# Performance work log

Hardware: AMD Instinct MI355X
Metric: run time of the kernel (lower is better)

## Reference

```python
import jax, jax.numpy as jnp
import numpy as np

B, T, C = 4, 1024, 1024
HS = 64
H = C // HS
D_W, D_A, D_V, D_G = 64, 64, 32, 128
EPS = 0.00064  # GroupNorm eps from the module


def _wkv(r, w, k, v, a, b):
    # RWKV-7 recurrence: S_t = S_{t-1}*diag(exp(-exp(w_t))) + (S_{t-1} a_t) b_t^T + v_t k_t^T ; y_t = S_t r_t
    Bv, Tv, Cv = r.shape
    rs = lambda t: t.reshape(Bv, Tv, H, HS)
    r, k, v, a, b = rs(r), rs(k), rs(v), rs(a), rs(b)
    wd = jnp.exp(-jnp.exp(rs(w)))  # per-head per-channel decay in (0,1)

    def step(S, xs):
        r_, w_, k_, v_, a_, b_ = xs  # each (B,H,N)
        sa = jnp.einsum('bhij,bhj->bhi', S, a_)
        S = S * w_[:, :, None, :] + sa[..., None] * b_[:, :, None, :] + v_[..., None] * k_[:, :, None, :]
        y = jnp.einsum('bhij,bhj->bhi', S, r_)
        return S, y

    xs = tuple(jnp.swapaxes(t, 0, 1) for t in (r, wd, k, v, a, b))  # (T,B,H,N)
    S0 = jnp.zeros((Bv, H, HS, HS), r.dtype)
    _, ys = jax.lax.scan(step, S0, xs)
    return jnp.swapaxes(ys, 0, 1).reshape(Bv, Tv, Cv)


def _forward(x, x_r, x_w, x_k, x_v, x_a, x_g, w0, w1, w2, a0, a1, a2, v0, v1, v2,
             g1, g2, k_k, k_a, r_k, Wr, Wk, Wv, Wo, ln_w, ln_b):
    Bv, Tv, Cv = x.shape
    # time_shift(x) - x  (ZeroPad2d((0,0,1,-1)))
    xx = jnp.concatenate([jnp.zeros_like(x[:, :1]), x[:, :-1]], axis=1) - x
    xr = x + xx * x_r; xw = x + xx * x_w; xk = x + xx * x_k
    xv = x + xx * x_v; xa = x + xx * x_a; xg = x + xx * x_g
    r = xr @ Wr
    w = -jax.nn.softplus(-(w0 + jnp.tanh(xw @ w1) @ w2)) - 0.5
    k = xk @ Wk
    v = xv @ Wv
    v_first = jax.lax.stop_gradient(v)  # first layer call: v_first == v.detach()
    v = v + (v_first - v) * jax.nn.sigmoid(v0 + xv @ v1 @ v2)
    a = jax.nn.sigmoid(a0 + xa @ a1 @ a2)
    g = jax.nn.sigmoid(xg @ g1) @ g2
    kk = k * k_k
    kkh = kk.reshape(Bv, Tv, H, HS)
    kkh = kkh / jnp.maximum(jnp.linalg.norm(kkh, axis=-1, keepdims=True), 1e-12)  # F.normalize
    kk = kkh.reshape(Bv, Tv, Cv)
    k = k * (1 + (a - 1) * k_a)
    y = _wkv(r, w, k, v, -kk, kk * a)
    # GroupNorm(H groups, eps=0.00064) over flattened (B*T, C)
    yh = y.reshape(Bv, Tv, H, HS)
    mu = jnp.mean(yh, axis=-1, keepdims=True)
    var = jnp.var(yh, axis=-1, keepdims=True)
    y = ((yh - mu) / jnp.sqrt(var + EPS)).reshape(Bv, Tv, Cv) * ln_w + ln_b
    rt = (r.reshape(Bv, Tv, H, HS) * k.reshape(Bv, Tv, H, HS) * r_k).sum(-1, keepdims=True) * v.reshape(Bv, Tv, H, HS)
    y = y + rt.reshape(Bv, Tv, Cv)
    return (y * g) @ Wo


def setup_inputs():
    key = jax.random.key(0)
    ks = jax.random.split(key, 28)
    it = iter(range(28))
    n = lambda shape, std: jax.random.normal(ks[next(it)], shape, jnp.float32) * std
    s = C ** -0.5
    return {
        'x': n((B, T, C), 1.0),
        'x_r': n((1, 1, C), 0.01), 'x_w': n((1, 1, C), 0.01), 'x_k': n((1, 1, C), 0.01),
        'x_v': n((1, 1, C), 0.01), 'x_a': n((1, 1, C), 0.01), 'x_g': n((1, 1, C), 0.01),
        'w0': n((1, 1, C), 0.02), 'w1': n((C, D_W), 0.04), 'w2': n((D_W, C), 0.04),
        'a0': n((1, 1, C), 0.02), 'a1': n((C, D_A), 0.04), 'a2': n((D_A, C), 0.04),
        'v0': n((1, 1, C), 0.02), 'v1': n((C, D_V), 0.04), 'v2': n((D_V, C), 0.04),
        'g1': n((C, D_G), 0.04), 'g2': n((D_G, C), 0.04),
        'k_k': n((1, 1, C), 0.02), 'k_a': n((1, 1, C), 0.02),
        'r_k': n((H, HS), 0.1) + 0.1 * jnp.arange(H, dtype=jnp.float32)[:, None],
        'Wr': n((C, C), s), 'Wk': n((C, C), s), 'Wv': n((C, C), s), 'Wo': n((C, C), s),
        'ln_w': jnp.ones((C,), jnp.float32), 'ln_b': jnp.zeros((C,), jnp.float32),
    }


def reference(x, x_r, x_w, x_k, x_v, x_a, x_g, w0, w1, w2, a0, a1, a2, v0, v1, v2,
              g1, g2, k_k, k_a, r_k, Wr, Wk, Wv, Wo, ln_w, ln_b):
    return _forward(x, x_r, x_w, x_k, x_v, x_a, x_g, w0, w1, w2, a0, a1, a2,
                    v0, v1, v2, g1, g2, k_k, k_a, r_k, Wr, Wk, Wv, Wo, ln_w, ln_b)
```

## Files before the change

kernel.cpp:

```cpp
#include <hip/hip_runtime.h>
#include <math.h>

#define Bsz 4
#define Tt  1024
#define Cc  1024
#define Hh  16
#define HSs 64
#define CL  32
#define NCH (Tt / CL)
#define STRD 260

typedef __attribute__((ext_vector_type(8))) short bf16x8;
typedef __attribute__((ext_vector_type(4))) float f32x4;

__device__ __forceinline__ float sigf(float x) { return 1.f / (1.f + expf(-x)); }

__device__ __forceinline__ unsigned short f2bf(float f) {
    unsigned int u = __float_as_uint(f);
    u = u + 0x7fffu + ((u >> 16) & 1u);
    return (unsigned short)(u >> 16);
}
__device__ __forceinline__ float bf2f(unsigned short u) {
    return __uint_as_float(((unsigned int)u) << 16);
}
__device__ __forceinline__ float dpp_add_xor1(float x) {
    int y = __builtin_amdgcn_mov_dpp(__float_as_int(x), 0xB1, 0xF, 0xF, true);
    return x + __int_as_float(y);
}
__device__ __forceinline__ float dpp_add_xor2(float x) {
    int y = __builtin_amdgcn_mov_dpp(__float_as_int(x), 0x4E, 0xF, 0xF, true);
    return x + __int_as_float(y);
}

__device__ __forceinline__ void gload16(const void* g, void* l) {
    __builtin_amdgcn_global_load_lds(
        (const __attribute__((address_space(1))) unsigned int*)g,
        (__attribute__((address_space(3))) unsigned int*)l, 16, 0, 0);
}

#define UNPK8(dst, u4, off) do { \
    const unsigned int* q_ = (const unsigned int*)&(u4); \
    _Pragma("unroll") \
    for (int e_ = 0; e_ < 4; ++e_) { \
        (dst)[(off) + 2 * e_]     = __uint_as_float(q_[e_] << 16); \
        (dst)[(off) + 2 * e_ + 1] = __uint_as_float(q_[e_] & 0xFFFF0000u); \
    } \
} while (0)

__device__ __forceinline__ void tcast64(
    const float* __restrict__ W, unsigned short* __restrict__ WT,
    int K, int N, int n0, int k0, int tid, unsigned short tile[64][68])
{
    const int tr = tid >> 4, tc4 = (tid & 15) * 4;
#pragma unroll
    for (int s = 0; s < 4; ++s) {
        int kk = tr + s * 16;
        float4 w4 = *(const float4*)(W + (size_t)(k0 + kk) * N + n0 + tc4);
        tile[kk][tc4 + 0] = f2bf(w4.x);
        tile[kk][tc4 + 1] = f2bf(w4.y);
        tile[kk][tc4 + 2] = f2bf(w4.z);
        tile[kk][tc4 + 3] = f2bf(w4.w);
    }
    __syncthreads();
#pragma unroll
    for (int s = 0; s < 4; ++s) {
        int nn = tr + s * 16;
        ushort4 o4;
        o4.x = tile[tc4 + 0][nn];
        o4.y = tile[tc4 + 1][nn];
        o4.z = tile[tc4 + 2][nn];
        o4.w = tile[tc4 + 3][nn];
        *(ushort4*)(WT + (size_t)(n0 + nn) * K + k0 + tc4) = o4;
    }
}

__global__ __launch_bounds__(256) void prep_all(
    const float* __restrict__ x, const float* __restrict__ x_r,
    const float* __restrict__ x_k, const float* __restrict__ x_v,
    const float* __restrict__ Wr, const float* __restrict__ Wk,
    const float* __restrict__ Wv, const float* __restrict__ Wo,
    const float* __restrict__ w1, const float* __restrict__ a1,
    const float* __restrict__ g1, const float* __restrict__ w2,
    const float* __restrict__ a2, const float* __restrict__ g2,
    unsigned short* __restrict__ xr, unsigned short* __restrict__ xk,
    unsigned short* __restrict__ xvo,
    unsigned short* __restrict__ WrT, unsigned short* __restrict__ WkT,
    unsigned short* __restrict__ WvT, unsigned short* __restrict__ WoT,
    unsigned short* __restrict__ w1t, unsigned short* __restrict__ a1t,
    unsigned short* __restrict__ g1t, unsigned short* __restrict__ w2t,
    unsigned short* __restrict__ a2t, unsigned short* __restrict__ g2t)
{
    __shared__ unsigned short tile[64][68];
    const int tid = threadIdx.x;
    int bid = blockIdx.x;

    if (bid < 4096) {
        const int row = bid;
        const int c0 = tid * 4;
        const size_t o = (size_t)row * Cc;
        float4 xc = *(const float4*)(x + o + c0);
        float4 xp;
        if (row & (Tt - 1)) xp = *(const float4*)(x + o - Cc + c0);
        else { xp.x = xp.y = xp.z = xp.w = 0.f; }
        float4 mr = *(const float4*)(x_r + c0);
        float4 mk = *(const float4*)(x_k + c0);
        float4 mv = *(const float4*)(x_v + c0);
        const float* xcf = (const float*)&xc; const float* xpf = (const float*)&xp;
        const float* mrf = (const float*)&mr; const float* mkf = (const float*)&mk;
        const float* mvf = (const float*)&mv;
        ushort4 r4, k4, v4;
        unsigned short* rp = (unsigned short*)&r4;
        unsigned short* kp = (unsigned short*)&k4;
        unsigned short* vp = (unsigned short*)&v4;
#pragma unroll
        for (int j = 0; j < 4; ++j) {
            float xx = xpf[j] - xcf[j];
            rp[j] = f2bf(xcf[j] + xx * mrf[j]);
            kp[j] = f2bf(xcf[j] + xx * mkf[j]);
            vp[j] = f2bf(xcf[j] + xx * mvf[j]);
        }
        *(ushort4*)(xr + o + c0) = r4;
        *(ushort4*)(xk + o + c0) = k4;
        *(ushort4*)(xvo + o + c0) = v4;
        return;
    }
    bid -= 4096;
    if (bid < 1024) {
        int which = bid >> 8, id0 = bid & 255;
        const float* W = which == 0 ? Wr : which == 1 ? Wk : which == 2 ? Wv : Wo;
        unsigned short* WT = which == 0 ? WrT : which == 1 ? WkT : which == 2 ? WvT : WoT;
        tcast64(W, WT, Cc, Cc, (id0 & 15) * 64, (id0 >> 4) * 64, tid, tile);
        return;
    }
    bid -= 1024;
    if (bid < 16) { tcast64(w1, w1t, Cc, 64, 0, bid * 64, tid, tile); return; }
    bid -= 16;
    if (bid < 16) { tcast64(a1, a1t, Cc, 64, 0, bid * 64, tid, tile); return; }
    bid -= 16;
    if (bid < 32) { tcast64(g1, g1t, Cc, 128, (bid & 1) * 64, (bid >> 1) * 64, tid, tile); return; }
    bid -= 32;
    if (bid < 16) { tcast64(w2, w2t, 64, Cc, bid * 64, 0, tid, tile); return; }
    bid -= 16;
    if (bid < 16) { tcast64(a2, a2t, 64, Cc, bid * 64, 0, tid, tile); return; }
    bid -= 16;
    tcast64(g2, g2t, 128, Cc, (bid & 15) * 64, (bid >> 4) * 64, tid, tile);
}

__global__ __launch_bounds__(256) void gemm_rkv(
    const unsigned short* __restrict__ xr, const unsigned short* __restrict__ xk,
    const unsigned short* __restrict__ xv,
    const unsigned short* __restrict__ WrT, const unsigned short* __restrict__ WkT,
    const unsigned short* __restrict__ WvT,
    unsigned short* __restrict__ rbh, unsigned short* __restrict__ kbh,
    unsigned short* __restrict__ vbh)
{
    const int z = blockIdx.z;
    const unsigned short* A  = z == 0 ? xr : z == 1 ? xk : xv;
    const unsigned short* WT = z == 0 ? WrT : z == 1 ? WkT : WvT;
    unsigned short* outh = z == 0 ? rbh : z == 1 ? kbh : vbh;
    const int K = Cc, N = Cc;

    const int bid = blockIdx.x + 8 * blockIdx.y;
    const int swz = (bid & 7) * 32 + (bid >> 3);
    const int row0 = (swz >> 3) * 128;
    const int col0 = (swz & 7) * 128;

    __shared__ __attribute__((aligned(16))) unsigned short As[128 * 32];
    __shared__ __attribute__((aligned(16))) unsigned short Bs[128 * 32];
    const int tid = threadIdx.x;
    const int wave = tid >> 6, lane = tid & 63;
    const int wr = wave >> 1, wc = wave & 1;
    const int lr = lane & 15, lk = lane >> 4;

    f32x4 acc[4][4];
#pragma unroll
    for (int m = 0; m < 4; ++m)
#pragma unroll
        for (int n = 0; n < 4; ++n)
#pragma unroll
            for (int r = 0; r < 4; ++r) acc[m][n][r] = 0.f;

    const int lrow = lane >> 2;
    const int lcol8 = (lane & 3) * 8;

    for (int k0 = 0; k0 < K; k0 += 32) {
#pragma unroll
        for (int e = 0; e < 2; ++e) {
            int cib = wave * 128 + e * 64;
            int row = (cib >> 2) + lrow;
            gload16(A  + (size_t)(row0 + row) * K + k0 + lcol8, &As[cib * 8]);
            gload16(WT + (size_t)(col0 + row) * K + k0 + lcol8, &Bs[cib * 8]);
        }
        __syncthreads();
        bf16x8 af[4], bff[4];
#pragma unroll
        for (int m = 0; m < 4; ++m)
            af[m] = *(const bf16x8*)&As[(wr * 64 + m * 16 + lr) * 32 + lk * 8];
#pragma unroll
        for (int n = 0; n < 4; ++n)
            bff[n] = *(const bf16x8*)&Bs[(wc * 64 + n * 16 + lr) * 32 + lk * 8];
#pragma unroll
        for (int m = 0; m < 4; ++m)
#pragma unroll
            for (int n = 0; n < 4; ++n)
                acc[m][n] = __builtin_amdgcn_mfma_f32_16x16x32_bf16(af[m], bff[n], acc[m][n], 0, 0, 0);
        __syncthreads();
    }

#pragma unroll
    for (int m = 0; m < 4; ++m)
#pragma unroll
        for (int n = 0; n < 4; ++n) {
            int col = col0 + wc * 64 + n * 16 + lr;
#pragma unroll
            for (int r = 0; r < 4; ++r) {
                int row = row0 + wr * 64 + m * 16 + lk * 4 + r;
                outh[(size_t)row * N + col] = f2bf(acc[m][n][r]);
            }
        }
}

__global__ __launch_bounds__(256) void gemm_bf16(
    const unsigned short* __restrict__ A, const unsigned short* __restrict__ WT,
    float* __restrict__ out, int M, int N, int K)
{
    __shared__ __attribute__((aligned(16))) unsigned short As[128 * 32];
    __shared__ __attribute__((aligned(16))) unsigned short Bs[128 * 32];
    const int bid = blockIdx.x + 8 * blockIdx.y;
    const int swz = (bid & 7) * 32 + (bid >> 3);
    const int row0 = (swz >> 3) * 128;
    const int col0 = (swz & 7) * 128;
    const int tid = threadIdx.x;
    const int wave = tid >> 6, lane = tid & 63;
    const int wr = wave >> 1, wc = wave & 1;
    const int lr = lane & 15, lk = lane >> 4;

    f32x4 acc[4][4];
#pragma unroll
    for (int m = 0; m < 4; ++m)
#pragma unroll
        for (int n = 0; n < 4; ++n)
#pragma unroll
            for (int r = 0; r < 4; ++r) acc[m][n][r] = 0.f;

    const int lrow = lane >> 2;
    const int lcol8 = (lane & 3) * 8;

    for (int k0 = 0; k0 < K; k0 += 32) {
#pragma unroll
        for (int e = 0; e < 2; ++e) {
            int cib = wave * 128 + e * 64;
            int row = (cib >> 2) + lrow;
            gload16(A  + (size_t)(row0 + row) * K + k0 + lcol8, &As[cib * 8]);
            gload16(WT + (size_t)(col0 + row) * K + k0 + lcol8, &Bs[cib * 8]);
        }
        __syncthreads();
        bf16x8 af[4], bff[4];
#pragma unroll
        for (int m = 0; m < 4; ++m)
            af[m] = *(const bf16x8*)&As[(wr * 64 + m * 16 + lr) * 32 + lk * 8];
#pragma unroll
        for (int n = 0; n < 4; ++n)
            bff[n] = *(const bf16x8*)&Bs[(wc * 64 + n * 16 + lr) * 32 + lk * 8];
#pragma unroll
        for (int m = 0; m < 4; ++m)
#pragma unroll
            for (int n = 0; n < 4; ++n)
                acc[m][n] = __builtin_amdgcn_mfma_f32_16x16x32_bf16(af[m], bff[n], acc[m][n], 0, 0, 0);
        __syncthreads();
    }

#pragma unroll
    for (int m = 0; m < 4; ++m)
#pragma unroll
        for (int n = 0; n < 4; ++n) {
            int col = col0 + wc * 64 + n * 16 + lr;
#pragma unroll
            for (int r = 0; r < 4; ++r) {
                int row = row0 + wr * 64 + m * 16 + lk * 4 + r;
                out[(size_t)row * N + col] = acc[m][n][r];
            }
        }
}

__global__ __launch_bounds__(256) void lowrank1_fused(
    const float* __restrict__ x,
    const float* __restrict__ x_w, const float* __restrict__ x_a,
    const float* __restrict__ x_g,
    const unsigned short* __restrict__ w1t, const unsigned short* __restrict__ a1t,
    const unsigned short* __restrict__ g1t,
    unsigned short* __restrict__ hw, unsigned short* __restrict__ ha,
    unsigned short* __restrict__ hg)
{
    const int seg = blockIdx.x;
    const float* mix; const unsigned short* WT; unsigned short* out;
    int N, col0, epi;
    if (seg == 0)      { mix = x_w; WT = w1t; out = hw; N = 64;  col0 = 0; epi = 1; }
    else if (seg == 1) { mix = x_a; WT = a1t; out = ha; N = 64;  col0 = 0; epi = 0; }
    else               { mix = x_g; WT = g1t; out = hg; N = 128; col0 = (seg - 2) * 64; epi = 2; }

    __shared__ __attribute__((aligned(16))) unsigned short As[64][40];
    __shared__ __attribute__((aligned(16))) unsigned short Bs[64][40];
    const int row0 = blockIdx.y * 64;
    const int tid = threadIdx.x;
    const int wave = tid >> 6, lane = tid & 63;
    const int lr = lane & 15, lk = lane >> 4;

    f32x4 acc[4];
#pragma unroll
    for (int n = 0; n < 4; ++n)
#pragma unroll
        for (int r = 0; r < 4; ++r) acc[n][r] = 0.f;

    for (int k0 = 0; k0 < Cc; k0 += 32) {
        {
            int ar = tid >> 2, ac = (tid & 3) * 8;
            int row = row0 + ar;
            const float* xp = x + (size_t)row * Cc + k0 + ac;
            float4 c0 = *(const float4*)xp;
            float4 c1 = *(const float4*)(xp + 4);
            float4 p0, p1;
            if (row & (Tt - 1)) {
                p0 = *(const float4*)(xp - Cc);
                p1 = *(const float4*)(xp - Cc + 4);
            } else {
                p0.x = p0.y = p0.z = p0.w = 0.f;
                p1.x = p1.y = p1.z = p1.w = 0.f;
            }
            float4 m0 = *(const float4*)(mix + k0 + ac);
            float4 m1 = *(const float4*)(mix + k0 + ac + 4);
            const float* cf0 = (const float*)&c0; const float* cf1 = (const float*)&c1;
            const float* pf0 = (const float*)&p0; const float* pf1 = (const float*)&p1;
            const float* mf0 = (const float*)&m0; const float* mf1 = (const float*)&m1;
            ushort4 u0, u1;
            unsigned short* up0 = (unsigned short*)&u0;
            unsigned short* up1 = (unsigned short*)&u1;
#pragma unroll
            for (int j = 0; j < 4; ++j) {
                up0[j] = f2bf(cf0[j] + (pf0[j] - cf0[j]) * mf0[j]);
                up1[j] = f2bf(cf1[j] + (pf1[j] - cf1[j]) * mf1[j]);
            }
            *(ushort4*)&As[ar][ac] = u0;
            *(ushort4*)&As[ar][ac + 4] = u1;
        }
        {
            int br = tid >> 2, bc = (tid & 3) * 8;
            *(uint4*)&Bs[br][bc] = *(const uint4*)(WT + (size_t)(col0 + br) * Cc + k0 + bc);
        }
        __syncthreads();
        bf16x8 af, bff[4];
        af = *(const bf16x8*)&As[wave * 16 + lr][lk * 8];
#pragma unroll
        for (int n = 0; n < 4; ++n)
            bff[n] = *(const bf16x8*)&Bs[n * 16 + lr][lk * 8];
#pragma unroll
        for (int n = 0; n < 4; ++n)
            acc[n] = __builtin_amdgcn_mfma_f32_16x16x32_bf16(af, bff[n], acc[n], 0, 0, 0);
        __syncthreads();
    }

#pragma unroll
    for (int n = 0; n < 4; ++n) {
        int col = col0 + n * 16 + lr;
#pragma unroll
        for (int r = 0; r < 4; ++r) {
            int row = row0 + wave * 16 + lk * 4 + r;
            float v = acc[n][r];
            if (epi == 1) v = tanhf(v);
            else if (epi == 2) v = sigf(v);
            out[(size_t)row * N + col] = f2bf(v);
        }
    }
}

__global__ __launch_bounds__(256) void stage2_fused(
    const unsigned short* __restrict__ hw, const unsigned short* __restrict__ ha,
    const unsigned short* __restrict__ hg,
    const unsigned short* __restrict__ w2t, const unsigned short* __restrict__ a2t,
    const unsigned short* __restrict__ g2t,
    unsigned short* __restrict__ wdbh, float* __restrict__ abf,
    unsigned short* __restrict__ gb,
    const float* __restrict__ w0, const float* __restrict__ a0)
{
    const int z = blockIdx.z;
    const unsigned short* A  = z == 0 ? hw : z == 1 ? ha : hg;
    const unsigned short* WT = z == 0 ? w2t : z == 1 ? a2t : g2t;
    const float* bias = z == 0 ? w0 : z == 1 ? a0 : nullptr;
    const int K = (z == 2) ? 128 : 64;
    const int N = Cc;

    __shared__ __attribute__((aligned(16))) unsigned short As[128 * 32];
    __shared__ __attribute__((aligned(16))) unsigned short Bs[64 * 32];
    const int row0 = blockIdx.y * 128;
    const int col0 = blockIdx.x * 64;
    const int tid = threadIdx.x;
    const int wave = tid >> 6, lane = tid & 63;
    const int lr = lane & 15, lk = lane >> 4;

    f32x4 acc[2][4];
#pragma unroll
    for (int m = 0; m < 2; ++m)
#pragma unroll
        for (int n = 0; n < 4; ++n)
#pragma unroll
            for (int r = 0; r < 4; ++r) acc[m][n][r] = 0.f;

    const int lrow = lane >> 2;
    const int lcol8 = (lane & 3) * 8;

    for (int k0 = 0; k0 < K; k0 += 32) {
#pragma unroll
        for (int e = 0; e < 2; ++e) {
            int cib = wave * 128 + e * 64;
            int row = (cib >> 2) + lrow;
            gload16(A + (size_t)(row0 + row) * K + k0 + lcol8, &As[cib * 8]);
        }
        {
            int cib = wave * 64;
            int row = (cib >> 2) + lrow;
            gload16(WT + (size_t)(col0 + row) * K + k0 + lcol8, &Bs[cib * 8]);
        }
        __syncthreads();
        bf16x8 af[2], bff[4];
#pragma unroll
        for (int m = 0; m < 2; ++m)
            af[m] = *(const bf16x8*)&As[(wave * 32 + m * 16 + lr) * 32 + lk * 8];
#pragma unroll
        for (int n = 0; n < 4; ++n)
            bff[n] = *(const bf16x8*)&Bs[(n * 16 + lr) * 32 + lk * 8];
#pragma unroll
        for (int m = 0; m < 2; ++m)
#pragma unroll
            for (int n = 0; n < 4; ++n)
                acc[m][n] = __builtin_amdgcn_mfma_f32_16x16x32_bf16(af[m], bff[n], acc[m][n], 0, 0, 0);
        __syncthreads();
    }

#pragma unroll
    for (int m = 0; m < 2; ++m)
#pragma unroll
        for (int n = 0; n < 4; ++n) {
            int col = col0 + n * 16 + lr;
#pragma unroll
            for (int r = 0; r < 4; ++r) {
                int row = row0 + wave * 32 + m * 16 + lk * 4 + r;
                float v = acc[m][n][r];
                if (bias) v += bias[col];
                if (z == 0) {
                    v = expf(-0.60653065971263342f * sigf(v));
                    wdbh[(size_t)row * N + col] = f2bf(v);
                } else if (z == 1) {
                    abf[(size_t)row * N + col] = sigf(v);
                } else {
                    gb[(size_t)row * N + col] = f2bf(v);
                }
            }
        }
}

__global__ __launch_bounds__(256, 1) void wkv_chunk1(
    const unsigned short* __restrict__ rbh, const unsigned short* __restrict__ wdbh,
    const unsigned short* __restrict__ kraw, const float* __restrict__ abf,
    const float* __restrict__ k_k, const float* __restrict__ k_a,
    unsigned short* __restrict__ TLt,
    unsigned short* __restrict__ Rho,
    unsigned short* __restrict__ ZLt,
    unsigned short* __restrict__ Alh)
{
    __shared__ float st[CL * STRD];
    __shared__ float A_l[CL][CL + 1];
    const int blk = blockIdx.x;
    const int bh = blk >> 5;
    const int c  = blk & (NCH - 1);
    const int b = bh >> 4, h = bh & 15;
    const size_t base = (size_t)b * Tt * Cc + h * HSs + (size_t)c * CL * Cc;
    const int tid = threadIdx.x;

    {
        const int s = tid >> 3, j8 = (tid & 7) * 8;
        const size_t go = base + (size_t)s * Cc + j8;
        {
            uint4 u = *(const uint4*)(wdbh + go);
            const unsigned int* q = (const unsigned int*)&u;
            float4 f0, f1;
            f0.x = __uint_as_float(q[0] << 16); f0.y = __uint_as_float(q[0] & 0xFFFF0000u);
            f0.z = __uint_as_float(q[1] << 16); f0.w = __uint_as_float(q[1] & 0xFFFF0000u);
            f1.x = __uint_as_float(q[2] << 16); f1.y = __uint_as_float(q[2] & 0xFFFF0000u);
            f1.z = __uint_as_float(q[3] << 16); f1.w = __uint_as_float(q[3] & 0xFFFF0000u);
            *(float4*)&st[s * STRD + 1 * 64 + j8] = f0;
            *(float4*)&st[s * STRD + 1 * 64 + j8 + 4] = f1;
        }
        {
            uint4 u = *(const uint4*)(rbh + go);
            const unsigned int* q = (const unsigned int*)&u;
            float4 f0, f1;
            f0.x = __uint_as_float(q[0] << 16); f0.y = __uint_as_float(q[0] & 0xFFFF0000u);
            f0.z = __uint_as_float(q[1] << 16); f0.w = __uint_as_float(q[1] & 0xFFFF0000u);
            f1.x = __uint_as_float(q[2] << 16); f1.y = __uint_as_float(q[2] & 0xFFFF0000u);
            f1.z = __uint_as_float(q[3] << 16); f1.w = __uint_as_float(q[3] & 0xFFFF0000u);
            *(float4*)&st[s * STRD + 3 * 64 + j8] = f0;
            *(float4*)&st[s * STRD + 3 * 64 + j8 + 4] = f1;
        }
        float kr[8];
        {
            uint4 u = *(const uint4*)(kraw + go);
            UNPK8(kr, u, 0);
        }
        float4 av0 = *(const float4*)(abf + go);
        float4 av1 = *(const float4*)(abf + go + 4);
        const float* avp0 = (const float*)&av0;
        const float* avp1 = (const float*)&av1;
        const int ch0 = h * HSs + j8;
        float4 kk0 = *(const float4*)(k_k + ch0);
        float4 kk1 = *(const float4*)(k_k + ch0 + 4);
        const float* kkw = (const float*)&kk0;
        const float* kkw1 = (const float*)&kk1;
        float kkv[8];
#pragma unroll
        for (int j = 0; j < 4; ++j) {
            kkv[j] = kr[j] * kkw[j];
            kkv[4 + j] = kr[4 + j] * kkw1[j];
        }
        float ssq = 0.f;
#pragma unroll
        for (int j = 0; j < 8; ++j) ssq = fmaf(kkv[j], kkv[j], ssq);
        ssq = dpp_add_xor1(ssq);
        ssq = dpp_add_xor2(ssq);
        ssq += __shfl_xor(ssq, 4);
        float inv = 1.f / fmaxf(sqrtf(ssq), 1e-12f);
        float4 aa0, aa1, bb0, bb1;
        float* aap = (float*)&aa0; float* bbp = (float*)&bb0;
#pragma unroll
        for (int j = 0; j < 4; ++j) {
            float kkn = kkv[j] * inv;
            aap[j] = -kkn;
            bbp[j] = kkn * avp0[j];
        }
        float* aq = (float*)&aa1; float* bq = (float*)&bb1;
#pragma unroll
        for (int j = 0; j < 4; ++j) {
            float kkn = kkv[4 + j] * inv;
            aq[j] = -kkn;
            bq[j] = kkn * avp1[j];
        }
        *(float4*)&st[s * STRD + 0 * 64 + j8] = aa0;
        *(float4*)&st[s * STRD + 0 * 64 + j8 + 4] = aa1;
        *(float4*)&st[s * STRD + 2 * 64 + j8] = bb0;
        *(float4*)&st[s * STRD + 2 * 64 + j8 + 4] = bb1;
    }
    __syncthreads();

    const int wv = tid >> 6, lane = tid & 63;
    if (wv < 2) {
        const int idx = wv * 64 + lane;
        const int rq = idx >> 2, jc = idx & 3;
        const int i0 = rq * 2, j0 = jc * 16;
        float T[2][16];
#pragma unroll
        for (int rr = 0; rr < 2; ++rr)
#pragma unroll
            for (int cc = 0; cc < 16; ++cc)
                T[rr][cc] = (i0 + rr == j0 + cc) ? 1.f : 0.f;
        const size_t rhob = (size_t)blk * (CL * 64);

        for (int t = 0; t < CL; ++t) {
            const float* sp = st + t * STRD;
            float a[16], w[16], bv[16], r[16];
#pragma unroll
            for (int q = 0; q < 4; ++q) {
                *(float4*)&a[q * 4]  = *(const float4*)(sp + 0 * 64 + j0 + q * 4);
                *(float4*)&w[q * 4]  = *(const float4*)(sp + 1 * 64 + j0 + q * 4);
                *(float4*)&bv[q * 4] = *(const float4*)(sp + 2 * 64 + j0 + q * 4);
                *(float4*)&r[q * 4]  = *(const float4*)(sp + 3 * 64 + j0 + q * 4);
            }
            float ta[2];
#pragma unroll
            for (int rr = 0; rr < 2; ++rr) {
                float q0 = T[rr][0] * a[0], q1 = T[rr][4] * a[4];
                float q2 = T[rr][8] * a[8], q3 = T[rr][12] * a[12];
#pragma unroll
                for (int e = 1; e < 4; ++e) {
                    q0 = fmaf(T[rr][e], a[e], q0);
                    q1 = fmaf(T[rr][4 + e], a[4 + e], q1);
                    q2 = fmaf(T[rr][8 + e], a[8 + e], q2);
                    q3 = fmaf(T[rr][12 + e], a[12 + e], q3);
                }
                ta[rr] = (q0 + q1) + (q2 + q3);
            }
#pragma unroll
            for (int rr = 0; rr < 2; ++rr) {
                ta[rr] = dpp_add_xor1(ta[rr]);
                ta[rr] = dpp_add_xor2(ta[rr]);
            }
            float rp[2];
#pragma unroll
            for (int rr = 0; rr < 2; ++rr) {
                float q0 = 0.f, q1 = 0.f, q2 = 0.f, q3 = 0.f;
#pragma unroll
                for (int e = 0; e < 4; ++e) {
                    T[rr][e]      = fmaf(T[rr][e],      w[e],      ta[rr] * bv[e]);
                    T[rr][4 + e]  = fmaf(T[rr][4 + e],  w[4 + e],  ta[rr] * bv[4 + e]);
                    T[rr][8 + e]  = fmaf(T[rr][8 + e],  w[8 + e],  ta[rr] * bv[8 + e]);
                    T[rr][12 + e] = fmaf(T[rr][12 + e], w[12 + e], ta[rr] * bv[12 + e]);
                    q0 = fmaf(T[rr][e], r[e], q0);
                    q1 = fmaf(T[rr][4 + e], r[4 + e], q1);
                    q2 = fmaf(T[rr][8 + e], r[8 + e], q2);
                    q3 = fmaf(T[rr][12 + e], r[12 + e], q3);
                }
                rp[rr] = (q0 + q1) + (q2 + q3);
            }
#pragma unroll
            for (int rr = 0; rr < 2; ++rr) {
                rp[rr] = dpp_add_xor1(rp[rr]);
                rp[rr] = dpp_add_xor2(rp[rr]);
            }
            if (jc == 0) {
                ushort2 o2;
                o2.x = f2bf(rp[0]); o2.y = f2bf(rp[1]);
                *(ushort2*)(Rho + rhob + t * 64 + i0) = o2;
            }
        }
        const size_t tlb = (size_t)blk * 4096;
#pragma unroll
        for (int cc = 0; cc < 16; ++cc) {
            ushort2 o2;
            o2.x = f2bf(T[0][cc]); o2.y = f2bf(T[1][cc]);
            *(ushort2*)(TLt + tlb + (size_t)(j0 + cc) * 64 + i0) = o2;
        }
    } else {
        const int idx2 = (wv - 2) * 64 + lane;
        const int s = idx2 >> 2, q4 = idx2 & 3;
        const int j0 = q4 * 16;
        float kreg[16];
        {
            float kr[16];
            uint4 u0 = *(const uint4*)(kraw + base + (size_t)s * Cc + j0);
            uint4 u1 = *(const uint4*)(kraw + base + (size_t)s * Cc + j0 + 8);
            UNPK8(kr, u0, 0); UNPK8(kr, u1, 8);
#pragma unroll
            for (int q = 0; q < 4; ++q) {
                float4 av4 = *(const float4*)(abf + base + (size_t)s * Cc + j0 + q * 4);
                float4 ka4 = *(const float4*)(k_a + h * HSs + j0 + q * 4);
                const float* avp = (const float*)&av4;
                const float* kap = (const float*)&ka4;
#pragma unroll
                for (int e = 0; e < 4; ++e) {
                    int u = q * 4 + e;
                    kreg[u] = kr[u] * (1.f + (avp[e] - 1.f) * kap[e]);
                }
            }
        }
        float z[16];
#pragma unroll
        for (int u = 0; u < 16; ++u) z[u] = 0.f;

        for (int t = 0; t < CL; ++t) {
            const float* sp = st + t * STRD;
            float a[16], w[16], bv[16], r[16];
#pragma unroll
            for (int q = 0; q < 4; ++q) {
                *(float4*)&a[q * 4]  = *(const float4*)(sp + 0 * 64 + j0 + q * 4);
                *(float4*)&w[q * 4]  = *(const float4*)(sp + 1 * 64 + j0 + q * 4);
                *(float4*)&bv[q * 4] = *(const float4*)(sp + 2 * 64 + j0 + q * 4);
                *(float4*)&r[q * 4]  = *(const float4*)(sp + 3 * 64 + j0 + q * 4);
            }
            float q0 = z[0] * a[0], q1 = z[4] * a[4];
            float q2 = z[8] * a[8], q3 = z[12] * a[12];
#pragma unroll
            for (int e = 1; e < 4; ++e) {
                q0 = fmaf(z[e], a[e], q0);
                q1 = fmaf(z[4 + e], a[4 + e], q1);
                q2 = fmaf(z[8 + e], a[8 + e], q2);
                q3 = fmaf(z[12 + e], a[12 + e], q3);
            }
            float za = (q0 + q1) + (q2 + q3);
            za = dpp_add_xor1(za);
            za = dpp_add_xor2(za);
#pragma unroll
            for (int u = 0; u < 16; ++u)
                z[u] = fmaf(z[u], w[u], za * bv[u]);
            if (s == t) {
#pragma unroll
                for (int u = 0; u < 16; ++u) z[u] = kreg[u];
            }
            float p0 = z[0] * r[0], p1 = z[4] * r[4];
            float p2 = z[8] * r[8], p3 = z[12] * r[12];
#pragma unroll
            for (int e = 1; e < 4; ++e) {
                p0 = fmaf(z[e], r[e], p0);
                p1 = fmaf(z[4 + e], r[4 + e], p1);
                p2 = fmaf(z[8 + e], r[8 + e], p2);
                p3 = fmaf(z[12 + e], r[12 + e], p3);
            }
            float al = (p0 + p1) + (p2 + p3);
            al = dpp_add_xor1(al);
            al = dpp_add_xor2(al);
            if (q4 == 0) A_l[t][s] = al;
        }
        const size_t zlb = (size_t)blk * (CL * 64);
#pragma unroll
        for (int u = 0; u < 16; ++u)
            ZLt[zlb + (size_t)(j0 + u) * 32 + s] = f2bf(z[u]);
    }
    __syncthreads();

    if (tid < 128) {
        const int t = tid >> 2, s8 = (tid & 3) * 8;
        ushort4 o0, o1;
        unsigned short* p0 = (unsigned short*)&o0;
        unsigned short* p1 = (unsigned short*)&o1;
#pragma unroll
        for (int e = 0; e < 4; ++e) {
            p0[e] = f2bf(A_l[t][s8 + e]);
            p1[e] = f2bf(A_l[t][s8 + 4 + e]);
        }
        unsigned short* dst = Alh + (size_t)blk * 1024 + t * 32 + s8;
        *(ushort4*)dst = o0;
        *(ushort4*)(dst + 4) = o1;
    }
}

__global__ __launch_bounds__(256, 1) void wkv_chunk2(
    const unsigned short* __restrict__ vbh, const unsigned short* __restrict__ TLt,
    const unsigned short* __restrict__ Rho, const unsigned short* __restrict__ ZLt,
    const unsigned short* __restrict__ Alh, float* __restrict__ yb)
{
    __shared__ unsigned short Sl[64 * 72];
    __shared__ unsigned short Ttl[64 * 72];
    __shared__ unsigned short Ztl[64 * 40];
    __shared__ unsigned short Rl[32 * 72];
    __shared__ unsigned short Vtl[64 * 40];
    __shared__ unsigned short All[32 * 40];
    const int bh = blockIdx.x;
    const size_t vbase = (size_t)(bh >> 4) * Tt * Cc + (bh & 15) * HSs;
    const int tid = threadIdx.x;
    const int wv = tid >> 6, lane = tid & 63;
    const int lr = lane & 15, lk = lane >> 4;
    const int i0w = wv * 16;

    f32x4 S[4];
#pragma unroll
    for (int n = 0; n < 4; ++n)
#pragma unroll
        for (int r = 0; r < 4; ++r) S[n][r] = 0.f;

    uint4 pT0, pT1, pZ, pR, pAl, pVu;
    const int vs = tid >> 3, vi0 = (tid & 7) * 8;

#define C2_LOAD(c_) do { \
    size_t cb_ = (size_t)(bh * NCH + (c_)); \
    const uint4* tp_ = (const uint4*)(TLt + cb_ * 4096); \
    pT0 = tp_[tid * 2]; pT1 = tp_[tid * 2 + 1]; \
    pZ = ((const uint4*)(ZLt + cb_ * 2048))[tid]; \
    pR = ((const uint4*)(Rho + cb_ * 2048))[tid]; \
    if (tid < 128) pAl = ((const uint4*)(Alh + cb_ * 1024))[tid]; \
    pVu = *(const uint4*)(vbh + vbase + (size_t)((c_) * CL + vs) * Cc + vi0); \
} while (0)

#define C2_STORE() do { \
    *(uint4*)&Ttl[(tid >> 2) * 72 + (tid & 3) * 16] = pT0; \
    *(uint4*)&Ttl[(tid >> 2) * 72 + (tid & 3) * 16 + 8] = pT1; \
    *(uint4*)&Ztl[(tid >> 2) * 40 + (tid & 3) * 8] = pZ; \
    *(uint4*)&Rl[(tid >> 3) * 72 + (tid & 7) * 8] = pR; \
    if (tid < 128) *(uint4*)&All[(tid >> 2) * 40 + (tid & 3) * 8] = pAl; \
    const unsigned short* pvu_ = (const unsigned short*)&pVu; \
    Vtl[(vi0 + 0) * 40 + vs] = pvu_[0]; \
    Vtl[(vi0 + 1) * 40 + vs] = pvu_[1]; \
    Vtl[(vi0 + 2) * 40 + vs] = pvu_[2]; \
    Vtl[(vi0 + 3) * 40 + vs] = pvu_[3]; \
    Vtl[(vi0 + 4) * 40 + vs] = pvu_[4]; \
    Vtl[(vi0 + 5) * 40 + vs] = pvu_[5]; \
    Vtl[(vi0 + 6) * 40 + vs] = pvu_[6]; \
    Vtl[(vi0 + 7) * 40 + vs] = pvu_[7]; \
} while (0)

    C2_LOAD(0);
    for (int c = 0; c < NCH; ++c) {
        __syncthreads();
#pragma unroll
        for (int n = 0; n < 4; ++n) {
#pragma unroll
            for (int r = 0; r < 4; ++r)
                Sl[(i0w + lk * 4 + r) * 72 + n * 16 + lr] = f2bf(S[n][r]);
        }
        C2_STORE();
        if (c + 1 < NCH) C2_LOAD(c + 1);
        __syncthreads();

        bf16x8 sA0 = *(const bf16x8*)&Sl[(i0w + lr) * 72 + lk * 8];
        bf16x8 sA1 = *(const bf16x8*)&Sl[(i0w + lr) * 72 + 32 + lk * 8];
        bf16x8 vA = *(const bf16x8*)&Vtl[(i0w + lr) * 40 + lk * 8];

#pragma unroll
        for (int nt = 0; nt < 2; ++nt) {
            int t = nt * 16 + lr;
            float* yp = yb + vbase + (size_t)(c * CL + t) * Cc + i0w + lk * 4;
            f32x4 yc = { 0.f, 0.f, 0.f, 0.f };
            bf16x8 b0 = *(const bf16x8*)&Rl[t * 72 + lk * 8];
            bf16x8 b1 = *(const bf16x8*)&Rl[t * 72 + 32 + lk * 8];
            bf16x8 al8 = *(const bf16x8*)&All[t * 40 + lk * 8];
            yc = __builtin_amdgcn_mfma_f32_16x16x32_bf16(sA0, b0, yc, 0, 0, 0);
            yc = __builtin_amdgcn_mfma_f32_16x16x32_bf16(sA1, b1, yc, 0, 0, 0);
            yc = __builtin_amdgcn_mfma_f32_16x16x32_bf16(vA, al8, yc, 0, 0, 0);
            *(f32x4*)yp = yc;
        }

#pragma unroll
        for (int n = 0; n < 4; ++n) {
            int j = n * 16 + lr;
            bf16x8 t0 = *(const bf16x8*)&Ttl[j * 72 + lk * 8];
            bf16x8 t1 = *(const bf16x8*)&Ttl[j * 72 + 32 + lk * 8];
            bf16x8 z0 = *(const bf16x8*)&Ztl[j * 40 + lk * 8];
            f32x4 acc = { 0.f, 0.f, 0.f, 0.f };
            acc = __builtin_amdgcn_mfma_f32_16x16x32_bf16(sA0, t0, acc, 0, 0, 0);
            acc = __builtin_amdgcn_mfma_f32_16x16x32_bf16(sA1, t1, acc, 0, 0, 0);
            acc = __builtin_amdgcn_mfma_f32_16x16x32_bf16(vA, z0, acc, 0, 0, 0);
            S[n] = acc;
        }
    }
#undef C2_LOAD
#undef C2_STORE
}

__global__ __launch_bounds__(256) void gn_rt_kernel(
    const float* __restrict__ yb, const unsigned short* __restrict__ rbh,
    const unsigned short* __restrict__ kraw, const float* __restrict__ abf,
    const unsigned short* __restrict__ vbh,
    const unsigned short* __restrict__ gb, const float* __restrict__ r_k,
    const float* __restrict__ k_a,
    const float* __restrict__ ln_w, const float* __restrict__ ln_b,
    unsigned short* __restrict__ zb)
{
    const int row = blockIdx.x;
    const int tid = threadIdx.x;
    const int c0 = tid * 4;
    const int hd = tid >> 4;
    const int n0 = c0 & 63;
    const size_t o = (size_t)row * Cc;

    float4 y4 = *(const float4*)(yb + o + c0);
    ushort4 r4u = *(const ushort4*)(rbh + o + c0);
    ushort4 k4u = *(const ushort4*)(kraw + o + c0);
    float4 a4 = *(const float4*)(abf + o + c0);
    ushort4 v4u = *(const ushort4*)(vbh + o + c0);
    ushort4 g4u = *(const ushort4*)(gb + o + c0);
    float4 rk4 = *(const float4*)(r_k + hd * 64 + n0);
    float4 ka4 = *(const float4*)(k_a + c0);

    float yv[4] = { y4.x, y4.y, y4.z, y4.w };
    float rv[4] = { bf2f(r4u.x), bf2f(r4u.y), bf2f(r4u.z), bf2f(r4u.w) };
    float krv[4] = { bf2f(k4u.x), bf2f(k4u.y), bf2f(k4u.z), bf2f(k4u.w) };
    const float* avp = (const float*)&a4;
    float vv[4] = { bf2f(v4u.x), bf2f(v4u.y), bf2f(v4u.z), bf2f(v4u.w) };
    float gv[4] = { bf2f(g4u.x), bf2f(g4u.y), bf2f(g4u.z), bf2f(g4u.w) };
    float rkv[4] = { rk4.x, rk4.y, rk4.z, rk4.w };
    const float* kap = (const float*)&ka4;

    float kv[4];
#pragma unroll
    for (int j = 0; j < 4; ++j)
        kv[j] = krv[j] * (1.f + (avp[j] - 1.f) * kap[j]);

    float sum = 0.f, ssq = 0.f, dot = 0.f;
#pragma unroll
    for (int j = 0; j < 4; ++j) {
        sum += yv[j];
        ssq += yv[j] * yv[j];
        dot += rv[j] * kv[j] * rkv[j];
    }
#pragma unroll
    for (int m = 1; m <= 8; m <<= 1) {
        sum += __shfl_xor(sum, m);
        ssq += __shfl_xor(ssq, m);
        dot += __shfl_xor(dot, m);
    }
    const float mu = sum * (1.f / 64.f);
    const float var = ssq * (1.f / 64.f) - mu * mu;
    const float inv = rsqrtf(var + 0.00064f);

    ushort4 z4;
    unsigned short* zp = (unsigned short*)&z4;
#pragma unroll
    for (int j = 0; j < 4; ++j) {
        int c = c0 + j;
        float yg = (yv[j] - mu) * inv * ln_w[c] + ln_b[c];
        yg += dot * vv[j];
        zp[j] = f2bf(yg * gv[j]);
    }
    *(ushort4*)(zb + o + c0) = z4;
}


extern "C" void kernel_launch(void* const* d_in, const int* in_sizes, int n_in,
                              void* d_out, int out_size, void* d_ws, size_t ws_size,
                              hipStream_t stream)
{
    const float* x   = (const float*)d_in[0];
    const float* x_r = (const float*)d_in[1];
    const float* x_w = (const float*)d_in[2];
    const float* x_k = (const float*)d_in[3];
    const float* x_v = (const float*)d_in[4];
    const float* x_a = (const float*)d_in[5];
    const float* x_g = (const float*)d_in[6];
    const float* w0  = (const float*)d_in[7];
    const float* w1  = (const float*)d_in[8];
    const float* w2  = (const float*)d_in[9];
    const float* a0  = (const float*)d_in[10];
    const float* a1  = (const float*)d_in[11];
    const float* a2  = (const float*)d_in[12];
    const float* g1  = (const float*)d_in[16];
    const float* g2  = (const float*)d_in[17];
    const float* k_k = (const float*)d_in[18];
    const float* k_a = (const float*)d_in[19];
    const float* r_k = (const float*)d_in[20];
    const float* Wr  = (const float*)d_in[21];
    const float* Wk  = (const float*)d_in[22];
    const float* Wv  = (const float*)d_in[23];
    const float* Wo  = (const float*)d_in[24];
    const float* ln_w = (const float*)d_in[25];
    const float* ln_b = (const float*)d_in[26];

    float* ws = (float*)d_ws;
    const size_t S = (size_t)Bsz * Tt * Cc;
    const int M = Bsz * Tt;

    unsigned short* rbh = (unsigned short*)(ws + 0 * S);
    unsigned short* zb  = (unsigned short*)ws + S;
    unsigned short* wdbh = (unsigned short*)(ws + 1 * S);
    unsigned short* gb  = (unsigned short*)(ws + 1 * S) + S;
    unsigned short* kbh = (unsigned short*)(ws + 2 * S);
    unsigned short* vbh = (unsigned short*)(ws + 2 * S) + S;
    float* abf = ws + 3 * S;
    float* yb = ws + 4 * S;
    unsigned short* xr = (unsigned short*)(ws + 5 * S);
    unsigned short* xk = (unsigned short*)(ws + 5 * S) + S;
    unsigned short* Rho = xr;
    unsigned short* ZLt = xk;
    unsigned short* xv = (unsigned short*)(ws + 6 * S);
    unsigned short* hw = xv + S;
    unsigned short* ha = hw + 262144;
    unsigned short* hg = ha + 262144;
    unsigned short* w1t = hg + 524288;
    unsigned short* a1t = w1t + 65536;
    unsigned short* g1t = a1t + 65536;
    unsigned short* w2t = g1t + 131072;
    unsigned short* a2t = w2t + 65536;
    unsigned short* g2t = a2t + 65536;
    unsigned short* WrT = (unsigned short*)(ws + 7 * S);
    unsigned short* WkT = WrT + 1048576;
    unsigned short* WvT = WkT + 1048576;
    unsigned short* WoT = WvT + 1048576;
    unsigned short* Alh = WoT + 1048576;
    unsigned short* TLt = (unsigned short*)(ws + 8 * S);

    dim3 blk(256);

    prep_all<<<dim3(4096 + 1024 + 128), blk, 0, stream>>>(
        x, x_r, x_k, x_v, Wr, Wk, Wv, Wo, w1, a1, g1, w2, a2, g2,
        xr, xk, xv, WrT, WkT, WvT, WoT, w1t, a1t, g1t, w2t, a2t, g2t);

    lowrank1_fused<<<dim3(4, 64), blk, 0, stream>>>(x, x_w, x_a, x_g, w1t, a1t, g1t, hw, ha, hg);

    gemm_rkv<<<dim3(8, 32, 3), blk, 0, stream>>>(xr, xk, xv, WrT, WkT, WvT, rbh, kbh, vbh);

    stage2_fused<<<dim3(16, 32, 3), blk, 0, stream>>>(hw, ha, hg, w2t, a2t, g2t, wdbh, abf, gb, w0, a0);

    wkv_chunk1<<<dim3(64 * NCH), dim3(256), 0, stream>>>(rbh, wdbh, kbh, abf, k_k, k_a, TLt, Rho, ZLt, Alh);
    wkv_chunk2<<<dim3(64), blk, 0, stream>>>(vbh, TLt, Rho, ZLt, Alh, yb);

    gn_rt_kernel<<<dim3(M), blk, 0, stream>>>(yb, rbh, kbh, abf, vbh, gb, r_k, k_a, ln_w, ln_b, zb);

    gemm_bf16<<<dim3(8, 32), blk, 0, stream>>>(zb, WoT, (float*)d_out, M, Cc, Cc);
}
```

Measured before the change: 225.2 us.

## Fuse GroupNorm and gating epilogue into the sequential WKV chunk kernel

The chunked WKV output is staged per chunk in shared memory and normalized in place. The GroupNorm, r*k*r_k bonus term and g gating are done inside wkv_chunk2, and the separate gn_rt kernel and the fp32 y buffer are removed. This saves a launch and a full fp32 write/read of y. The cost is that each of the 32 sequential chunk steps now does extra global loads of r, k, a, g and v plus an added barrier. That is work on the latency-bound critical path of a 64-block kernel.

```diff
diff --git a/kernel.cpp b/kernel.cpp
--- a/kernel.cpp
+++ b/kernel.cpp
@@ -723,7 +723,12 @@
 __global__ __launch_bounds__(256, 1) void wkv_chunk2(
     const unsigned short* __restrict__ vbh, const unsigned short* __restrict__ TLt,
     const unsigned short* __restrict__ Rho, const unsigned short* __restrict__ ZLt,
-    const unsigned short* __restrict__ Alh, float* __restrict__ yb)
+    const unsigned short* __restrict__ Alh,
+    const unsigned short* __restrict__ rbh, const unsigned short* __restrict__ kraw,
+    const float* __restrict__ abf, const unsigned short* __restrict__ gb,
+    const float* __restrict__ r_k, const float* __restrict__ k_a,
+    const float* __restrict__ ln_w, const float* __restrict__ ln_b,
+    unsigned short* __restrict__ zb)
 {
     __shared__ unsigned short Sl[64 * 72];
     __shared__ unsigned short Ttl[64 * 72];
@@ -731,8 +736,10 @@
     __shared__ unsigned short Rl[32 * 72];
     __shared__ unsigned short Vtl[64 * 40];
     __shared__ unsigned short All[32 * 40];
+    __shared__ float Yl[32 * 68];
     const int bh = blockIdx.x;
-    const size_t vbase = (size_t)(bh >> 4) * Tt * Cc + (bh & 15) * HSs;
+    const int h = bh & 15;
+    const size_t vbase = (size_t)(bh >> 4) * Tt * Cc + h * HSs;
     const int tid = threadIdx.x;
     const int wv = tid >> 6, lane = tid & 63;
     const int lr = lane & 15, lk = lane >> 4;
@@ -743,6 +750,19 @@
     for (int n = 0; n < 4; ++n)
 #pragma unroll
         for (int r = 0; r < 4; ++r) S[n][r] = 0.f;
+
+    const int gt = tid >> 3;
+    const int gi = (tid & 7) * 8;
+    const int chb = h * HSs + gi;
+    float ka8[8], rk8[8], lnw8[8], lnb8[8];
+    *(float4*)&ka8[0] = *(const float4*)(k_a + chb);
+    *(float4*)&ka8[4] = *(const float4*)(k_a + chb + 4);
+    *(float4*)&rk8[0] = *(const float4*)(r_k + chb);
+    *(float4*)&rk8[4] = *(const float4*)(r_k + chb + 4);
+    *(float4*)&lnw8[0] = *(const float4*)(ln_w + chb);
+    *(float4*)&lnw8[4] = *(const float4*)(ln_w + chb + 4);
+    *(float4*)&lnb8[0] = *(const float4*)(ln_b + chb);
+    *(float4*)&lnb8[4] = *(const float4*)(ln_b + chb + 4);
 
     uint4 pT0, pT1, pZ, pR, pAl, pVu;
     const int vs = tid >> 3, vi0 = (tid & 7) * 8;
@@ -794,7 +814,6 @@
 #pragma unroll
         for (int nt = 0; nt < 2; ++nt) {
             int t = nt * 16 + lr;
-            float* yp = yb + vbase + (size_t)(c * CL + t) * Cc + i0w + lk * 4;
             f32x4 yc = { 0.f, 0.f, 0.f, 0.f };
             bf16x8 b0 = *(const bf16x8*)&Rl[t * 72 + lk * 8];
             bf16x8 b1 = *(const bf16x8*)&Rl[t * 72 + 32 + lk * 8];
@@ -802,7 +821,7 @@
             yc = __builtin_amdgcn_mfma_f32_16x16x32_bf16(sA0, b0, yc, 0, 0, 0);
             yc = __builtin_amdgcn_mfma_f32_16x16x32_bf16(sA1, b1, yc, 0, 0, 0);
             yc = __builtin_amdgcn_mfma_f32_16x16x32_bf16(vA, al8, yc, 0, 0, 0);
-            *(f32x4*)yp = yc;
+            *(float4*)&Yl[t * 68 + i0w + lk * 4] = *(float4*)&yc;
         }
 
 #pragma unroll
@@ -817,77 +836,55 @@
             acc = __builtin_amdgcn_mfma_f32_16x16x32_bf16(vA, z0, acc, 0, 0, 0);
             S[n] = acc;
         }
+
+        __syncthreads();
+
+        {
+            const size_t grow = vbase + (size_t)(c * CL + gt) * Cc + gi;
+            float y8[8];
+            *(float4*)&y8[0] = *(const float4*)&Yl[gt * 68 + gi];
+            *(float4*)&y8[4] = *(const float4*)&Yl[gt * 68 + gi + 4];
+            float r8[8], k8[8], g8[8], v8[8];
+            uint4 ur = *(const uint4*)(rbh + grow);  UNPK8(r8, ur, 0);
+            uint4 uk = *(const uint4*)(kraw + grow); UNPK8(k8, uk, 0);
+            uint4 ug = *(const uint4*)(gb + grow);   UNPK8(g8, ug, 0);
+            uint4 uv = *(const uint4*)(vbh + grow);  UNPK8(v8, uv, 0);
+            float a8[8];
+            *(float4*)&a8[0] = *(const float4*)(abf + grow);
+            *(float4*)&a8[4] = *(const float4*)(abf + grow + 4);
+
+            float sum = 0.f, ssq = 0.f, dot = 0.f;
+            float kf8[8];
+#pragma unroll
+            for (int j = 0; j < 8; ++j) {
+                kf8[j] = k8[j] * (1.f + (a8[j] - 1.f) * ka8[j]);
+                sum += y8[j];
+                ssq = fmaf(y8[j], y8[j], ssq);
+                dot = fmaf(r8[j] * kf8[j], rk8[j], dot);
+            }
+            sum = dpp_add_xor1(sum); sum = dpp_add_xor2(sum); sum += __shfl_xor(sum, 4);
+            ssq = dpp_add_xor1(ssq); ssq = dpp_add_xor2(ssq); ssq += __shfl_xor(ssq, 4);
+            dot = dpp_add_xor1(dot); dot = dpp_add_xor2(dot); dot += __shfl_xor(dot, 4);
+            const float mu = sum * (1.f / 64.f);
+            const float var = ssq * (1.f / 64.f) - mu * mu;
+            const float inv = rsqrtf(var + 0.00064f);
+
+            ushort4 z0o, z1o;
+            unsigned short* zp0 = (unsigned short*)&z0o;
+            unsigned short* zp1 = (unsigned short*)&z1o;
+#pragma unroll
+            for (int j = 0; j < 4; ++j) {
+                float yg0 = (y8[j] - mu) * inv * lnw8[j] + lnb8[j] + dot * v8[j];
+                float yg1 = (y8[4 + j] - mu) * inv * lnw8[4 + j] + lnb8[4 + j] + dot * v8[4 + j];
+                zp0[j] = f2bf(yg0 * g8[j]);
+                zp1[j] = f2bf(yg1 * g8[4 + j]);
+            }
+            *(ushort4*)(zb + grow) = z0o;
+            *(ushort4*)(zb + grow + 4) = z1o;
+        }
     }
 #undef C2_LOAD
 #undef C2_STORE
-}
-
-__global__ __launch_bounds__(256) void gn_rt_kernel(
-    const float* __restrict__ yb, const unsigned short* __restrict__ rbh,
-    const unsigned short* __restrict__ kraw, const float* __restrict__ abf,
-    const unsigned short* __restrict__ vbh,
-    const unsigned short* __restrict__ gb, const float* __restrict__ r_k,
-    const float* __restrict__ k_a,
-    const float* __restrict__ ln_w, const float* __restrict__ ln_b,
-    unsigned short* __restrict__ zb)
-{
-    const int row = blockIdx.x;
-    const int tid = threadIdx.x;
-    const int c0 = tid * 4;
-    const int hd = tid >> 4;
-    const int n0 = c0 & 63;
-    const size_t o = (size_t)row * Cc;
-
-    float4 y4 = *(const float4*)(yb + o + c0);
-    ushort4 r4u = *(const ushort4*)(rbh + o + c0);
-    ushort4 k4u = *(const ushort4*)(kraw + o + c0);
-    float4 a4 = *(const float4*)(abf + o + c0);
-    ushort4 v4u = *(const ushort4*)(vbh + o + c0);
-    ushort4 g4u = *(const ushort4*)(gb + o + c0);
-    float4 rk4 = *(const float4*)(r_k + hd * 64 + n0);
-    float4 ka4 = *(const float4*)(k_a + c0);
-
-    float yv[4] = { y4.x, y4.y, y4.z, y4.w };
-    float rv[4] = { bf2f(r4u.x), bf2f(r4u.y), bf2f(r4u.z), bf2f(r4u.w) };
-    float krv[4] = { bf2f(k4u.x), bf2f(k4u.y), bf2f(k4u.z), bf2f(k4u.w) };
-    const float* avp = (const float*)&a4;
-    float vv[4] = { bf2f(v4u.x), bf2f(v4u.y), bf2f(v4u.z), bf2f(v4u.w) };
-    float gv[4] = { bf2f(g4u.x), bf2f(g4u.y), bf2f(g4u.z), bf2f(g4u.w) };
-    float rkv[4] = { rk4.x, rk4.y, rk4.z, rk4.w };
-    const float* kap = (const float*)&ka4;
-
-    float kv[4];
-#pragma unroll
-    for (int j = 0; j < 4; ++j)
-        kv[j] = krv[j] * (1.f + (avp[j] - 1.f) * kap[j]);
-
-    float sum = 0.f, ssq = 0.f, dot = 0.f;
-#pragma unroll
-    for (int j = 0; j < 4; ++j) {
-        sum += yv[j];
-        ssq += yv[j] * yv[j];
-        dot += rv[j] * kv[j] * rkv[j];
-    }
-#pragma unroll
-    for (int m = 1; m <= 8; m <<= 1) {
-        sum += __shfl_xor(sum, m);
-        ssq += __shfl_xor(ssq, m);
-        dot += __shfl_xor(dot, m);
-    }
-    const float mu = sum * (1.f / 64.f);
-    const float var = ssq * (1.f / 64.f) - mu * mu;
-    const float inv = rsqrtf(var + 0.00064f);
-
-    ushort4 z4;
-    unsigned short* zp = (unsigned short*)&z4;
-#pragma unroll
-    for (int j = 0; j < 4; ++j) {
-        int c = c0 + j;
-        float yg = (yv[j] - mu) * inv * ln_w[c] + ln_b[c];
-        yg += dot * vv[j];
-        zp[j] = f2bf(yg * gv[j]);
-    }
-    *(ushort4*)(zb + o + c0) = z4;
 }
 
 
@@ -931,7 +928,6 @@
     unsigned short* kbh = (unsigned short*)(ws + 2 * S);
     unsigned short* vbh = (unsigned short*)(ws + 2 * S) + S;
     float* abf = ws + 3 * S;
-    float* yb = ws + 4 * S;
     unsigned short* xr = (unsigned short*)(ws + 5 * S);
     unsigned short* xk = (unsigned short*)(ws + 5 * S) + S;
     unsigned short* Rho = xr;
@@ -966,9 +962,8 @@
     stage2_fused<<<dim3(16, 32, 3), blk, 0, stream>>>(hw, ha, hg, w2t, a2t, g2t, wdbh, abf, gb, w0, a0);
 
     wkv_chunk1<<<dim3(64 * NCH), dim3(256), 0, stream>>>(rbh, wdbh, kbh, abf, k_k, k_a, TLt, Rho, ZLt, Alh);
-    wkv_chunk2<<<dim3(64), blk, 0, stream>>>(vbh, TLt, Rho, ZLt, Alh, yb);
-
-    gn_rt_kernel<<<dim3(M), blk, 0, stream>>>(yb, rbh, kbh, abf, vbh, gb, r_k, k_a, ln_w, ln_b, zb);
+    wkv_chunk2<<<dim3(64), blk, 0, stream>>>(vbh, TLt, Rho, ZLt, Alh,
+                                             rbh, kbh, abf, gb, r_k, k_a, ln_w, ln_b, zb);
 
     gemm_bf16<<<dim3(8, 32), blk, 0, stream>>>(zb, WoT, (float*)d_out, M, Cc, Cc);
 }
```

New measurement: 239.2 us. 1.06x slower.
